# Optimization experiments

Hardware: AMD Instinct MI355X
Metric: run time of the kernel (lower is better)

Reference implementation:

```python
import jax, jax.numpy as jnp
import numpy as np

B, CIN, NF, COUT, H, W = 128, 64, 16, 256, 20, 20


def _warp(features, f):
    # features: (B, Cin, r, c), f: (r, c, 2) flow offsets
    r, c = features.shape[2], features.shape[3]
    grid = jnp.stack(
        jnp.meshgrid(jnp.arange(r, dtype=f.dtype), jnp.arange(c, dtype=f.dtype), indexing='ij'),
        axis=-1,
    )  # (r, c, 2) base index map
    idx = grid + f  # index_map += inverse, inverse == flow[i] after double negation
    base = jnp.floor(idx)
    frac = jax.lax.stop_gradient(idx - base)  # torch detaches s and t
    s, t = frac[..., 0], frac[..., 1]
    b = base.astype(jnp.int32)
    bx, by = b[..., 0], b[..., 1]
    padded = jnp.pad(features, ((0, 0), (0, 0), (1, 1), (1, 1)))  # zero pad by 1

    def gather(ix, iy):
        cx = jnp.clip(ix, 0, r)
        cy = jnp.clip(iy, 0, c)
        return padded[:, :, cx + 1, cy + 1]  # (B, Cin, r, c)

    # NOTE: weight for base_10 is s*(1-t) in the original source (apparent bug,
    # should be (1-s)*t) -- replicated here for faithfulness.
    w00 = (1 - s) * (1 - t)
    w01 = s * (1 - t)
    w10 = s * (1 - t)
    w11 = s * t
    return (gather(bx, by) * w00 + gather(bx + 1, by) * w01
            + gather(bx, by + 1) * w10 + gather(bx + 1, by + 1) * w11)


def setup_inputs() -> dict:
    key = jax.random.key(0)
    k1, k2, k3, k4 = jax.random.split(key, 4)
    x = jax.random.normal(k1, (B, CIN, H, W), dtype=jnp.float32)
    flow = jax.random.normal(k2, (NF, H, W, 2), dtype=jnp.float32)
    combinator = jax.random.normal(k3, (COUT, CIN * NF), dtype=jnp.float32) / np.sqrt(CIN * NF)
    bias = jax.random.normal(k4, (COUT,), dtype=jnp.float32) / np.sqrt(CIN * NF)
    return {"x": x, "flow": flow, "combinator": combinator, "bias": bias}


def reference(x, flow, combinator, bias):
    # per-flow bilinear warp, vectorized over the flow axis
    warped = jax.vmap(lambda f: _warp(x, f))(flow)  # (nf, B, Cin, h, w)
    nf, b, cin, h, w = warped.shape
    # permute(1,3,4,2,0).reshape -> columns ordered channel-major, flow-minor
    feat = warped.transpose(1, 3, 4, 2, 0).reshape(b, h, w, cin * nf)
    out = jnp.einsum('bhwk,ok->bhwo', feat, combinator) + bias
    return out.transpose(0, 3, 1, 2)  # (B, Cout, h, w)
```

## Files before the change

kernel.cpp:

```cpp
#include <hip/hip_runtime.h>
#include <hip/hip_fp16.h>
#include <stdint.h>

#define BATCH 128
#define CIN   64
#define NFLOW 16
#define COUT  256
#define HH    20
#define WW    20
#define NPIX  400
#define KTOT  1024
#define PT    80
#define NPT   5
#define NTH   512
#define FLS   72

typedef __attribute__((ext_vector_type(8))) short sh8;
typedef __attribute__((ext_vector_type(4))) float f4;

__global__ void prep_w(const float* __restrict__ wg, __half* __restrict__ Wf) {
    int gid = blockIdx.x * 256 + threadIdx.x;
    int j8  = gid & 127;
    int row = gid >> 7;
    int kc16 = j8 >> 2;
    int h    = j8 & 3;
    __half* dst = Wf + ((size_t)(kc16 * 16 + (row >> 4)) * 64 + h * 16 + (row & 15)) * 8;
    #pragma unroll
    for (int j = 0; j < 8; ++j) {
        int kp = j8 * 8 + j;
        int kc = kp >> 6;
        int l  = kp & 63;
        int f  = (kc >> 3) * 8 + (l >> 3);
        int c  = (kc & 7) * 8 + (l & 7);
        dst[j] = __float2half(wg[(size_t)row * KTOT + c * NFLOW + f]);
    }
}

__global__ __launch_bounds__(NTH, 4) void flow_main(
    const float* __restrict__ xg, const __half* __restrict__ Wf,
    const float* __restrict__ flowg, const float* __restrict__ biasg,
    float* __restrict__ outg)
{
    __shared__ __align__(16) __half xb[CIN * NPIX];
    __shared__ __align__(16) __half fl[2][PT * FLS];

    const int bid0 = blockIdx.x;
    const int bid  = (bid0 & 7) * (BATCH * NPT / 8) + (bid0 >> 3);
    const int b  = bid / NPT;
    const int pt = bid - b * NPT;
    const int p0 = pt * PT;

    const int tid  = threadIdx.x;
    const int wv   = tid >> 6;
    const int lane = tid & 63;
    const int lr   = lane & 15;
    const int lk   = (lane >> 4) * 8;

    const float* xsrc = xg + (size_t)b * (CIN * NPIX);

    #pragma unroll
    for (int it = 0; it < 7; ++it) {
        int idx = it * NTH + tid;
        if (idx < 3200) {
            int cb  = idx / NPIX;
            int pix = idx - cb * NPIX;
            const float* s = xsrc + (size_t)(cb * 8) * NPIX + pix;
            __half2 h0 = __floats2half2_rn(s[0 * NPIX], s[1 * NPIX]);
            __half2 h1 = __floats2half2_rn(s[2 * NPIX], s[3 * NPIX]);
            __half2 h2 = __floats2half2_rn(s[4 * NPIX], s[5 * NPIX]);
            __half2 h3 = __floats2half2_rn(s[6 * NPIX], s[7 * NPIX]);
            uint4 pk;
            pk.x = __builtin_bit_cast(uint32_t, h0);
            pk.y = __builtin_bit_cast(uint32_t, h1);
            pk.z = __builtin_bit_cast(uint32_t, h2);
            pk.w = __builtin_bit_cast(uint32_t, h3);
            *(uint4*)&xb[(size_t)idx * 8] = pk;
        }
    }

    __half2 w2_[2][4];
    int     pb_[2][4];
    int     fo_[2];

    auto build_tables = [&](int fb) {
        #pragma unroll
        for (int it = 0; it < 2; ++it) {
            if (it == 0 || lane < 16) {
                int p  = it * 64 + lane;
                int f  = fb * 8 + wv;
                int gp = p0 + p;
                int i = gp / WW;
                int j = gp - i * WW;
                float fx = flowg[((f * HH + i) * WW + j) * 2 + 0];
                float fy = flowg[((f * HH + i) * WW + j) * 2 + 1];
                float ax = (float)i + fx;
                float ay = (float)j + fy;
                float bxf = floorf(ax), byf = floorf(ay);
                float s = ax - bxf, t = ay - byf;
                int ibx = (int)bxf, iby = (int)byf;
                float w00 = (1.f - s) * (1.f - t);
                float w01 = s * (1.f - t);
                float w10 = s * (1.f - t);
                float w11 = s * t;
                int cx0 = min(max(ibx, 0), HH);
                int cx1 = min(max(ibx + 1, 0), HH);
                int cy0 = min(max(iby, 0), WW);
                int cy1 = min(max(iby + 1, 0), WW);
                int v0 = (cx0 < HH) & (cy0 < WW);
                int v1 = (cx1 < HH) & (cy0 < WW);
                int v2 = (cx0 < HH) & (cy1 < WW);
                int v3 = (cx1 < HH) & (cy1 < WW);
                w2_[it][0] = __half2half2(__float2half(v0 ? w00 : 0.f));
                w2_[it][1] = __half2half2(__float2half(v1 ? w01 : 0.f));
                w2_[it][2] = __half2half2(__float2half(v2 ? w10 : 0.f));
                w2_[it][3] = __half2half2(__float2half(v3 ? w11 : 0.f));
                pb_[it][0] = (v0 ? (cx0 * WW + cy0) : 0) * 16;
                pb_[it][1] = (v1 ? (cx1 * WW + cy0) : 0) * 16;
                pb_[it][2] = (v2 ? (cx0 * WW + cy1) : 0) * 16;
                pb_[it][3] = (v3 ? (cx1 * WW + cy1) : 0) * 16;
                fo_[it] = p * (FLS * 2) + wv * 16;
            }
        }
    };

    auto fill = [&](int kc) {
        const char* xcb = (const char*)xb + (kc & 7) * 6400;
        char* flb = (char*)fl[kc & 1];
        #pragma unroll
        for (int it = 0; it < 2; ++it) {
            if (it == 0 || lane < 16) {
                __half2 s0 = __builtin_bit_cast(__half2, 0u);
                __half2 s1 = s0, s2 = s0, s3 = s0;
                #pragma unroll
                for (int q = 0; q < 4; ++q) {
                    const uint4 d = *(const uint4*)(xcb + pb_[it][q]);
                    __half2 wq = w2_[it][q];
                    s0 = __hfma2(wq, __builtin_bit_cast(__half2, d.x), s0);
                    s1 = __hfma2(wq, __builtin_bit_cast(__half2, d.y), s1);
                    s2 = __hfma2(wq, __builtin_bit_cast(__half2, d.z), s2);
                    s3 = __hfma2(wq, __builtin_bit_cast(__half2, d.w), s3);
                }
                uint4 pk;
                pk.x = __builtin_bit_cast(uint32_t, s0);
                pk.y = __builtin_bit_cast(uint32_t, s1);
                pk.z = __builtin_bit_cast(uint32_t, s2);
                pk.w = __builtin_bit_cast(uint32_t, s3);
                *(uint4*)(flb + fo_[it]) = pk;
            }
        }
    };

    build_tables(0);
    __syncthreads();
    fill(0);
    __syncthreads();

    f4 acc[2][5] = {};

    for (int kc = 0; kc < 16; ++kc) {
        if (kc == 7) build_tables(1);

        const sh8* wfp = (const sh8*)Wf + (size_t)(2 * kc * 16 + 2 * wv) * 64 + lane;
        sh8 a00 = wfp[0];
        sh8 a01 = wfp[64];
        sh8 a10 = wfp[1024];
        sh8 a11 = wfp[1088];

        if (kc < 15) fill(kc + 1);

        const __half* flr = fl[kc & 1];
        __builtin_amdgcn_s_setprio(1);
        #pragma unroll
        for (int nf = 0; nf < 5; ++nf) {
            sh8 b0 = *(const sh8*)&flr[(nf * 16 + lr) * FLS + lk];
            acc[0][nf] = __builtin_amdgcn_mfma_f32_16x16x32_f16(a00, b0, acc[0][nf], 0, 0, 0);
            acc[1][nf] = __builtin_amdgcn_mfma_f32_16x16x32_f16(a01, b0, acc[1][nf], 0, 0, 0);
            sh8 b1 = *(const sh8*)&flr[(nf * 16 + lr) * FLS + 32 + lk];
            acc[0][nf] = __builtin_amdgcn_mfma_f32_16x16x32_f16(a10, b1, acc[0][nf], 0, 0, 0);
            acc[1][nf] = __builtin_amdgcn_mfma_f32_16x16x32_f16(a11, b1, acc[1][nf], 0, 0, 0);
        }
        __builtin_amdgcn_s_setprio(0);

        __syncthreads();
    }

    float* ob = outg + (size_t)b * (COUT * NPIX) + p0;
    #pragma unroll
    for (int mi = 0; mi < 2; ++mi) {
        #pragma unroll
        for (int r = 0; r < 4; ++r) {
            int m = (wv * 2 + mi) * 16 + (lane >> 4) * 4 + r;
            float bs = biasg[m];
            #pragma unroll
            for (int nf = 0; nf < 5; ++nf)
                ob[(size_t)m * NPIX + nf * 16 + lr] = acc[mi][nf][r] + bs;
        }
    }
}

extern "C" void kernel_launch(void* const* d_in, const int* in_sizes, int n_in,
                              void* d_out, int out_size, void* d_ws, size_t ws_size,
                              hipStream_t stream) {
    const float* x    = (const float*)d_in[0];
    const float* flow = (const float*)d_in[1];
    const float* comb = (const float*)d_in[2];
    const float* bias = (const float*)d_in[3];
    float* out = (float*)d_out;

    __half* Wf = (__half*)d_ws;

    prep_w<<<dim3(128), dim3(256), 0, stream>>>(comb, Wf);
    flow_main<<<dim3(BATCH * NPT), dim3(NTH), 0, stream>>>(x, Wf, flow, bias, out);
}
```

Before: 55.62 us.

## Pre-transpose x to fp16 pixel-major and stream channel chunks via LDS DMA

Adds a prep_x kernel that converts x to fp16 in a pixel-major, channel-minor layout in the workspace. The main kernel then stops holding the whole per-batch feature map in LDS. Instead it double-buffers 8-channel slices with global_load_lds, issued two steps ahead of the warp/fill stage. This cuts LDS use, raising the launch-bounds occupancy hint from 4 to 6, and replaces the in-kernel fp32 load and convert prologue with an overlapped stream. The cost is an extra kernel launch with strided reads, extra loads of padding rows past 400 pixels, and reliance on barriers to make the async LDS copies visible.

Result: slower. 103.9 us (+86.9%).

```diff
diff --git a/kernel.cpp b/kernel.cpp
--- a/kernel.cpp
+++ b/kernel.cpp
@@ -14,6 +14,7 @@
 #define NPT   5
 #define NTH   512
 #define FLS   72
+#define XCC   448
 
 typedef __attribute__((ext_vector_type(8))) short sh8;
 typedef __attribute__((ext_vector_type(4))) float f4;
@@ -36,12 +37,25 @@
     }
 }
 
-__global__ __launch_bounds__(NTH, 4) void flow_main(
-    const float* __restrict__ xg, const __half* __restrict__ Wf,
+__global__ void prep_x(const float* __restrict__ xg, __half* __restrict__ xt) {
+    int bid  = blockIdx.x;
+    int b    = bid >> 2, q = bid & 3;
+    int lane = threadIdx.x & 63;
+    int w    = threadIdx.x >> 6;
+    const float* src = xg + (size_t)b * (CIN * NPIX) + (size_t)lane * NPIX;
+    __half*      dst = xt + (size_t)b * (NPIX * CIN) + lane;
+    int pbeg = q * 100 + w * 25;
+    #pragma unroll
+    for (int p = pbeg; p < pbeg + 25; ++p)
+        dst[(size_t)p * CIN] = __float2half(src[p]);
+}
+
+__global__ __launch_bounds__(NTH, 6) void flow_main(
+    const __half* __restrict__ xt, const __half* __restrict__ Wf,
     const float* __restrict__ flowg, const float* __restrict__ biasg,
     float* __restrict__ outg)
 {
-    __shared__ __align__(16) __half xb[CIN * NPIX];
+    __shared__ __align__(16) __half xc[2][XCC * 8];
     __shared__ __align__(16) __half fl[2][PT * FLS];
 
     const int bid0 = blockIdx.x;
@@ -56,27 +70,17 @@
     const int lr   = lane & 15;
     const int lk   = (lane >> 4) * 8;
 
-    const float* xsrc = xg + (size_t)b * (CIN * NPIX);
-
-    #pragma unroll
-    for (int it = 0; it < 7; ++it) {
-        int idx = it * NTH + tid;
-        if (idx < 3200) {
-            int cb  = idx / NPIX;
-            int pix = idx - cb * NPIX;
-            const float* s = xsrc + (size_t)(cb * 8) * NPIX + pix;
-            __half2 h0 = __floats2half2_rn(s[0 * NPIX], s[1 * NPIX]);
-            __half2 h1 = __floats2half2_rn(s[2 * NPIX], s[3 * NPIX]);
-            __half2 h2 = __floats2half2_rn(s[4 * NPIX], s[5 * NPIX]);
-            __half2 h3 = __floats2half2_rn(s[6 * NPIX], s[7 * NPIX]);
-            uint4 pk;
-            pk.x = __builtin_bit_cast(uint32_t, h0);
-            pk.y = __builtin_bit_cast(uint32_t, h1);
-            pk.z = __builtin_bit_cast(uint32_t, h2);
-            pk.w = __builtin_bit_cast(uint32_t, h3);
-            *(uint4*)&xb[(size_t)idx * 8] = pk;
-        }
-    }
+    const __half* xtb = xt + (size_t)b * (NPIX * CIN);
+
+    auto stage_x = [&](int k) {
+        if (wv < 7) {
+            const __half* src = xtb + (size_t)(wv * 64 + lane) * CIN + (k & 7) * 8;
+            __builtin_amdgcn_global_load_lds(
+                (const __attribute__((address_space(1))) void*)src,
+                (__attribute__((address_space(3))) void*)&xc[k & 1][wv * 64 * 8],
+                16, 0, 0);
+        }
+    };
 
     __half2 w2_[2][4];
     int     pb_[2][4];
@@ -123,9 +127,9 @@
         }
     };
 
-    auto fill = [&](int kc) {
-        const char* xcb = (const char*)xb + (kc & 7) * 6400;
-        char* flb = (char*)fl[kc & 1];
+    auto fill = [&](int k) {
+        const char* xcb = (const char*)xc[k & 1];
+        char* flb = (char*)fl[k & 1];
         #pragma unroll
         for (int it = 0; it < 2; ++it) {
             if (it == 0 || lane < 16) {
@@ -151,6 +155,8 @@
     };
 
     build_tables(0);
+    stage_x(0);
+    stage_x(1);
     __syncthreads();
     fill(0);
     __syncthreads();
@@ -166,7 +172,9 @@
         sh8 a10 = wfp[1024];
         sh8 a11 = wfp[1088];
 
-        if (kc < 15) fill(kc + 1);
+        if (kc <= 13) stage_x(kc + 2);
+
+        if (kc <= 14) fill(kc + 1);
 
         const __half* flr = fl[kc & 1];
         __builtin_amdgcn_s_setprio(1);
@@ -208,7 +216,9 @@
     float* out = (float*)d_out;
 
     __half* Wf = (__half*)d_ws;
+    __half* xt = (__half*)((char*)d_ws + (512 << 10));
 
     prep_w<<<dim3(128), dim3(256), 0, stream>>>(comb, Wf);
-    flow_main<<<dim3(BATCH * NPT), dim3(NTH), 0, stream>>>(x, Wf, flow, bias, out);
-}
+    prep_x<<<dim3(512), dim3(256), 0, stream>>>(x, xt);
+    flow_main<<<dim3(BATCH * NPT), dim3(NTH), 0, stream>>>(xt, Wf, flow, bias, out);
+}
```

## Enlarge pixel tile to 100 and XOR-swizzle the LDS B-operand layout

Applied to the files above, without the earlier changes.

Each block now handles 100 pixels instead of 80, so each batch needs 4 tiles rather than 5. That cuts the block count and how often each block must reload and convert x into shared memory. The flow-feature LDS buffer drops row padding in favour of a 128-byte row with an XOR swizzle on 16-byte chunks, to avoid bank conflicts on the MFMA B reads. In exchange, the MFMA loop runs 7 n-fragments (112 columns), so 12 padded columns are computed and then discarded, and the epilogue gains a store mask.

After: 49.25 us. -11.5%, faster.

```diff
diff --git a/kernel.cpp b/kernel.cpp
--- a/kernel.cpp
+++ b/kernel.cpp
@@ -10,10 +10,11 @@
 #define WW    20
 #define NPIX  400
 #define KTOT  1024
-#define PT    80
-#define NPT   5
+#define PT    100
+#define NPT   4
 #define NTH   512
-#define FLS   72
+#define NFR   7
+#define FLR   112
 
 typedef __attribute__((ext_vector_type(8))) short sh8;
 typedef __attribute__((ext_vector_type(4))) float f4;
@@ -42,19 +43,19 @@
     float* __restrict__ outg)
 {
     __shared__ __align__(16) __half xb[CIN * NPIX];
-    __shared__ __align__(16) __half fl[2][PT * FLS];
+    __shared__ __align__(16) __half fl[2][FLR * 64];
 
     const int bid0 = blockIdx.x;
-    const int bid  = (bid0 & 7) * (BATCH * NPT / 8) + (bid0 >> 3);
-    const int b  = bid / NPT;
-    const int pt = bid - b * NPT;
+    const int bid  = (bid0 & 7) * 64 + (bid0 >> 3);
+    const int b  = bid >> 2;
+    const int pt = bid & 3;
     const int p0 = pt * PT;
 
     const int tid  = threadIdx.x;
     const int wv   = tid >> 6;
     const int lane = tid & 63;
     const int lr   = lane & 15;
-    const int lk   = (lane >> 4) * 8;
+    const int hq   = lane >> 4;
 
     const float* xsrc = xg + (size_t)b * (CIN * NPIX);
 
@@ -85,7 +86,7 @@
     auto build_tables = [&](int fb) {
         #pragma unroll
         for (int it = 0; it < 2; ++it) {
-            if (it == 0 || lane < 16) {
+            if (it == 0 || lane < PT - 64) {
                 int p  = it * 64 + lane;
                 int f  = fb * 8 + wv;
                 int gp = p0 + p;
@@ -118,17 +119,17 @@
                 pb_[it][1] = (v1 ? (cx1 * WW + cy0) : 0) * 16;
                 pb_[it][2] = (v2 ? (cx0 * WW + cy1) : 0) * 16;
                 pb_[it][3] = (v3 ? (cx1 * WW + cy1) : 0) * 16;
-                fo_[it] = p * (FLS * 2) + wv * 16;
+                fo_[it] = p * 128 + ((wv ^ (p & 7)) << 4);
             }
         }
     };
 
-    auto fill = [&](int kc) {
-        const char* xcb = (const char*)xb + (kc & 7) * 6400;
-        char* flb = (char*)fl[kc & 1];
+    auto fill = [&](int k) {
+        const char* xcb = (const char*)xb + (k & 7) * 6400;
+        char* flb = (char*)fl[k & 1];
         #pragma unroll
         for (int it = 0; it < 2; ++it) {
-            if (it == 0 || lane < 16) {
+            if (it == 0 || lane < PT - 64) {
                 __half2 s0 = __builtin_bit_cast(__half2, 0u);
                 __half2 s1 = s0, s2 = s0, s3 = s0;
                 #pragma unroll
@@ -155,7 +156,9 @@
     fill(0);
     __syncthreads();
 
-    f4 acc[2][5] = {};
+    f4 acc[2][NFR] = {};
+
+    const int q0 = (hq ^ (lr & 7)) << 4;
 
     for (int kc = 0; kc < 16; ++kc) {
         if (kc == 7) build_tables(1);
@@ -166,16 +169,17 @@
         sh8 a10 = wfp[1024];
         sh8 a11 = wfp[1088];
 
-        if (kc < 15) fill(kc + 1);
-
-        const __half* flr = fl[kc & 1];
+        if (kc <= 14) fill(kc + 1);
+
+        const char* flr_b = (const char*)fl[kc & 1];
         __builtin_amdgcn_s_setprio(1);
         #pragma unroll
-        for (int nf = 0; nf < 5; ++nf) {
-            sh8 b0 = *(const sh8*)&flr[(nf * 16 + lr) * FLS + lk];
+        for (int nf = 0; nf < NFR; ++nf) {
+            int rowb = (nf * 16 + lr) * 128;
+            sh8 b0 = *(const sh8*)(flr_b + (rowb + q0));
             acc[0][nf] = __builtin_amdgcn_mfma_f32_16x16x32_f16(a00, b0, acc[0][nf], 0, 0, 0);
             acc[1][nf] = __builtin_amdgcn_mfma_f32_16x16x32_f16(a01, b0, acc[1][nf], 0, 0, 0);
-            sh8 b1 = *(const sh8*)&flr[(nf * 16 + lr) * FLS + 32 + lk];
+            sh8 b1 = *(const sh8*)(flr_b + ((rowb + q0) ^ 64));
             acc[0][nf] = __builtin_amdgcn_mfma_f32_16x16x32_f16(a10, b1, acc[0][nf], 0, 0, 0);
             acc[1][nf] = __builtin_amdgcn_mfma_f32_16x16x32_f16(a11, b1, acc[1][nf], 0, 0, 0);
         }
@@ -189,11 +193,13 @@
     for (int mi = 0; mi < 2; ++mi) {
         #pragma unroll
         for (int r = 0; r < 4; ++r) {
-            int m = (wv * 2 + mi) * 16 + (lane >> 4) * 4 + r;
+            int m = (wv * 2 + mi) * 16 + hq * 4 + r;
             float bs = biasg[m];
             #pragma unroll
-            for (int nf = 0; nf < 5; ++nf)
-                ob[(size_t)m * NPIX + nf * 16 + lr] = acc[mi][nf][r] + bs;
+            for (int nf = 0; nf < NFR; ++nf) {
+                if (nf < 6 || lr < 4)
+                    ob[(size_t)m * NPIX + nf * 16 + lr] = acc[mi][nf][r] + bs;
+            }
         }
     }
 }
```
